# Optimization experiments

Measured on AMD Instinct MI355X. Metric: run time of the kernel, lower is better.

## Reference

```python
import jax, jax.numpy as jnp
import numpy as np

B, ST, SK, D, H, HD, MLP, BLK, NRAND = 2, 2048, 2048, 512, 8, 64, 2048, 64, 3


def _bigbird_block_mask(nq, nk, r, rng):
    """Block-level BigBird mask: 3-block window + global first/last blocks + r random blocks/row."""
    bm = np.zeros((nq, nk), dtype=bool)
    for i in range(nq):
        bm[i, max(i - 1, 0):min(i + 2, nk)] = True  # sliding window of 3 blocks
    bm[0, :] = True; bm[-1, :] = True              # global query blocks
    bm[:, 0] = True; bm[:, -1] = True              # global key blocks
    for i in range(nq):
        avail = np.where(~bm[i])[0]
        if avail.size:
            bm[i, rng.choice(avail, size=min(r, avail.size), replace=False)] = True
    return bm


def _masks():
    rng = np.random.RandomState(0)  # connectivity_seed = 0
    nb_q, nb_k = ST // BLK, SK // BLK
    self_bm = _bigbird_block_mask(nb_q, nb_q, NRAND, rng)
    cross_bm = _bigbird_block_mask(nb_q, nb_k, NRAND, rng)
    ones_blk = np.ones((BLK, BLK), dtype=bool)
    self_mask = np.kron(self_bm, ones_blk) & np.tril(np.ones((ST, ST), dtype=bool))  # causal self-attn
    cross_mask = np.kron(cross_bm, ones_blk)
    return jnp.asarray(self_mask), jnp.asarray(cross_mask)


def setup_inputs() -> dict:
    key = jax.random.key(0)
    ks = jax.random.split(key, 12)
    sd = np.float32(1.0 / np.sqrt(D))
    sh = np.float32(1.0 / np.sqrt(H * HD))
    sm = np.float32(1.0 / np.sqrt(MLP))
    self_mask, cross_mask = _masks()
    return dict(
        targets=jax.random.normal(ks[0], (B, ST, D), jnp.float32),
        encoded=jax.random.normal(ks[1], (B, SK, D), jnp.float32),
        ln1_scale=jnp.ones((D,), jnp.float32), ln1_bias=jnp.zeros((D,), jnp.float32),
        ln2_scale=jnp.ones((D,), jnp.float32), ln2_bias=jnp.zeros((D,), jnp.float32),
        ln3_scale=jnp.ones((D,), jnp.float32), ln3_bias=jnp.zeros((D,), jnp.float32),
        wq1=jax.random.normal(ks[2], (D, H, HD), jnp.float32) * sd,
        wk1=jax.random.normal(ks[3], (D, H, HD), jnp.float32) * sd,
        wv1=jax.random.normal(ks[4], (D, H, HD), jnp.float32) * sd,
        wo1=jax.random.normal(ks[5], (H, HD, D), jnp.float32) * sh,
        wq2=jax.random.normal(ks[6], (D, H, HD), jnp.float32) * sd,
        wk2=jax.random.normal(ks[7], (D, H, HD), jnp.float32) * sd,
        wv2=jax.random.normal(ks[8], (D, H, HD), jnp.float32) * sd,
        wo2=jax.random.normal(ks[9], (H, HD, D), jnp.float32) * sh,
        mlp_w1=jax.random.normal(ks[10], (D, MLP), jnp.float32) * sd,
        mlp_b1=jnp.zeros((MLP,), jnp.float32),
        mlp_w2=jax.random.normal(ks[11], (MLP, D), jnp.float32) * sm,
        mlp_b2=jnp.zeros((D,), jnp.float32),
        self_mask=self_mask, cross_mask=cross_mask,
    )


def _ln(x, s, b, eps=1e-6):
    mu = jnp.mean(x, axis=-1, keepdims=True)
    var = jnp.mean(jnp.square(x - mu), axis=-1, keepdims=True)
    return (x - mu) * jax.lax.rsqrt(var + eps) * s + b


def _attn(xq, xkv, wq, wk, wv, wo, mask):
    q = jnp.einsum('bsd,dhk->bshk', xq, wq) * np.float32(1.0 / np.sqrt(HD))
    k = jnp.einsum('bsd,dhk->bshk', xkv, wk)
    v = jnp.einsum('bsd,dhk->bshk', xkv, wv)
    scores = jnp.einsum('bqhd,bkhd->bhqk', q, k)
    scores = jnp.where(mask[None, None], scores, jnp.float32(-1e9))
    w = jax.nn.softmax(scores, axis=-1)
    o = jnp.einsum('bhqk,bkhd->bqhd', w, v)
    return jnp.einsum('bqhd,hdo->bqo', o, wo)


def reference(targets, encoded, ln1_scale, ln1_bias, ln2_scale, ln2_bias, ln3_scale, ln3_bias,
              wq1, wk1, wv1, wo1, wq2, wk2, wv2, wo2,
              mlp_w1, mlp_b1, mlp_w2, mlp_b2, self_mask, cross_mask):
    # causal BigBird self-attention + residual
    x = _ln(targets, ln1_scale, ln1_bias)
    x = _attn(x, x, wq1, wk1, wv1, wo1, self_mask) + targets
    # BigBird cross-attention over encoder output + residual
    y = _ln(x, ln2_scale, ln2_bias)
    y = _attn(y, encoded, wq2, wk2, wv2, wo2, cross_mask) + x
    # MLP block + residual
    z = _ln(y, ln3_scale, ln3_bias)
    z = jax.nn.gelu(z @ mlp_w1 + mlp_b1) @ mlp_w2 + mlp_b2
    return y + z
```

## Files before the change

kernel.cpp:

```cpp
#include <hip/hip_runtime.h>
#include <hip/hip_bf16.h>

#define DEVINL __device__ __forceinline__

namespace {

constexpr int kB = 2, kST = 2048, kSK = 2048, kD = 512, kH = 8, kHD = 64, kMLP = 2048, kBLK = 64;
constexpr int kNBQ = kST / kBLK;
constexpr int kNBK = kSK / kBLK;
constexpr int kROWS = kB * kST;

typedef float f32x4 __attribute__((ext_vector_type(4)));
typedef int i32x4 __attribute__((ext_vector_type(4)));
typedef short bf16x8 __attribute__((ext_vector_type(8)));

DEVINL float bf2f(unsigned short u) { return __uint_as_float(((unsigned)u) << 16); }

DEVINL unsigned short f2bf(float f) {
  __hip_bfloat16 h = __float2bfloat16(f);
  return *reinterpret_cast<unsigned short*>(&h);
}

DEVINL f32x4 mfma16(bf16x8 a, bf16x8 b, f32x4 c) {
  return __builtin_amdgcn_mfma_f32_16x16x32_bf16(a, b, c, 0, 0, 0);
}

DEVINL int swzb(int r) { return (((r & 7) ^ ((r >> 3) & 7)) << 4); }

__global__ __launch_bounds__(256) void tobf_kernel(const void* __restrict__ src, unsigned short* __restrict__ dst,
                                                   int n8, const unsigned* __restrict__ probe) {
  const bool bf = (probe[0] == 0x3F803F80u);
  const int stride = gridDim.x * blockDim.x;
  if (bf) {
    const i32x4* s = (const i32x4*)src;
    i32x4* d = (i32x4*)dst;
    for (int i = blockIdx.x * blockDim.x + threadIdx.x; i < n8; i += stride) d[i] = s[i];
  } else {
    const f32x4* s = (const f32x4*)src;
    i32x4* d = (i32x4*)dst;
    for (int i = blockIdx.x * blockDim.x + threadIdx.x; i < n8; i += stride) {
      const f32x4 a = s[2 * i], c = s[2 * i + 1];
      union { i32x4 v; unsigned short u[8]; } pk;
#pragma unroll
      for (int j = 0; j < 4; j++) { pk.u[j] = f2bf(a[j]); pk.u[4 + j] = f2bf(c[j]); }
      d[i] = pk.v;
    }
  }
}

struct PSrc { const void* s[8]; };
__global__ __launch_bounds__(256) void param_cvt_kernel(PSrc ps, float* __restrict__ dst,
                                                        const unsigned* __restrict__ probe) {
  const bool bf = (probe[0] == 0x3F803F80u);
  const int i = blockIdx.x * blockDim.x + threadIdx.x;
  if (i >= 5632) return;
  int seg, off;
  if (i < 3072) { seg = i >> 9; off = i & 511; }
  else if (i < 5120) { seg = 6; off = i - 3072; }
  else { seg = 7; off = i - 5120; }
  dst[i] = bf ? bf2f(((const unsigned short*)ps.s[seg])[off]) : ((const float*)ps.s[seg])[off];
}

struct TDesc { const void* src; unsigned short* dst; int K, N, start; float alpha; };
struct TPack { TDesc d[10]; };

__global__ __launch_bounds__(256) void transpose_batch_kernel(TPack p, const unsigned* __restrict__ probe) {
  __shared__ float tile[32][33];
  const bool bf = (probe[0] == 0x3F803F80u);
  const int bid = blockIdx.x;
  int di = 0;
#pragma unroll
  for (int i = 1; i < 10; i++)
    if (bid >= p.d[i].start) di = i;
  const TDesc dd = p.d[di];
  const int local = bid - dd.start;
  const int gx = dd.N / 32;
  const int bx = (local % gx) * 32;
  const int by = (local / gx) * 32;
  const int tx = threadIdx.x & 31, ty = threadIdx.x >> 5;
#pragma unroll
  for (int j = 0; j < 4; j++) {
    const int kr = by + ty + j * 8;
    float v;
    if (bf) v = bf2f(((const unsigned short*)dd.src)[(size_t)kr * dd.N + bx + tx]);
    else v = ((const float*)dd.src)[(size_t)kr * dd.N + bx + tx];
    tile[ty + j * 8][tx] = v;
  }
  __syncthreads();
#pragma unroll
  for (int j = 0; j < 4; j++) {
    const int nr = bx + ty + j * 8;
    dd.dst[(size_t)nr * dd.K + by + tx] = f2bf(dd.alpha * tile[tx][ty + j * 8]);
  }
}

DEVINL int mask_fmt(const void* self_mask) {
  const unsigned* sw = (const unsigned*)self_mask;
  unsigned w = sw[32256];
  unsigned w0 = sw[0];
  if (w == 0x01010101u) return 0;
  if (w0 == 0x3F800000u) return 2;
  if (w0 == 0x00003F80u) return 3;
  return 1;
}

DEVINL bool mask_at(const void* m, int r, int c, int fmt) {
  size_t idx = (size_t)r * kSK + c;
  switch (fmt) {
    case 0: return ((const unsigned char*)m)[idx] != 0;
    case 2: return ((const float*)m)[idx] != 0.f;
    case 3: return ((const unsigned short*)m)[idx] != 0;
    default: return ((const int*)m)[idx] != 0;
  }
}

__global__ void mask_kernel(const void* __restrict__ smask, const void* __restrict__ cmask,
                            unsigned char* __restrict__ sbm, unsigned char* __restrict__ cbm) {
  int fmt = mask_fmt(smask);
  int t = blockIdx.x * blockDim.x + threadIdx.x;
  if (t < kNBQ * kNBK) {
    int i = t / kNBK, j = t % kNBK;
    sbm[t] = mask_at(smask, i * kBLK + kBLK - 1, j * kBLK, fmt) ? 1 : 0;
    cbm[t] = mask_at(cmask, i * kBLK, j * kBLK, fmt) ? 1 : 0;
  }
}

__global__ __launch_bounds__(256) void ln_kernel(const void* __restrict__ x, const float* __restrict__ s,
                                                 const float* __restrict__ b, unsigned short* __restrict__ out,
                                                 int raw, const unsigned* __restrict__ probe) {
  const int row = blockIdx.x, t = threadIdx.x;
  float v0, v1;
  if (raw && probe[0] == 0x3F803F80u) {
    const unsigned u = ((const unsigned*)x)[(size_t)row * 256 + t];
    v0 = bf2f((unsigned short)u);
    v1 = bf2f((unsigned short)(u >> 16));
  } else {
    const float2 f = ((const float2*)x)[(size_t)row * 256 + t];
    v0 = f.x; v1 = f.y;
  }
  float sum = v0 + v1;
#pragma unroll
  for (int o = 32; o; o >>= 1) sum += __shfl_xor(sum, o);
  __shared__ float red[4], red2[4];
  const int wid = t >> 6, lane = t & 63;
  if (lane == 0) red[wid] = sum;
  __syncthreads();
  const float mu = (red[0] + red[1] + red[2] + red[3]) * (1.f / 512.f);
  float d0 = v0 - mu, d1 = v1 - mu;
  float vs = d0 * d0 + d1 * d1;
#pragma unroll
  for (int o = 32; o; o >>= 1) vs += __shfl_xor(vs, o);
  if (lane == 0) red2[wid] = vs;
  __syncthreads();
  const float rstd = rsqrtf((red2[0] + red2[1] + red2[2] + red2[3]) * (1.f / 512.f) + 1e-6f);
  const float o0 = d0 * rstd * s[2 * t] + b[2 * t];
  const float o1 = d1 * rstd * s[2 * t + 1] + b[2 * t + 1];
  ((unsigned*)out)[(size_t)row * 256 + t] = (unsigned)f2bf(o0) | ((unsigned)f2bf(o1) << 16);
}

DEVINL float gelu_f(float x) {
  float u = 0.7978845608028654f * (x + 0.044715f * x * x * x);
  return 0.5f * x * (1.f + tanhf(u));
}

enum { GEPI_QKV = 0, GEPI_BF16 = 1, GEPI_RESID_RAW = 2, GEPI_RESID = 3, GEPI_GELU = 4, GEPI_FINAL = 5 };

template <int BM, int WM, int WN, int MT, int NT, int EPI>
__global__ __launch_bounds__(256) void mfma_gemm_kernel(
    const unsigned short* __restrict__ A, const unsigned short* __restrict__ Bt,
    void* __restrict__ Cout, int M, int N, int K,
    const float* __restrict__ bias, const void* __restrict__ resid,
    const unsigned* __restrict__ probe) {
  __shared__ __align__(16) unsigned short As[2][BM * 64];
  __shared__ __align__(16) unsigned short Bs[2][128 * 64];
  const int t = threadIdx.x, w = t >> 6, lane = t & 63;
  const int lg = lane >> 4, lc = lane & 15;
  const int wm = w / WN, wn = w % WN;
  const int bm = blockIdx.y * BM, bn = blockIdx.x * 128;

  f32x4 acc[MT][NT];
#pragma unroll
  for (int mt = 0; mt < MT; mt++)
#pragma unroll
    for (int nt = 0; nt < NT; nt++) acc[mt][nt] = f32x4{0.f, 0.f, 0.f, 0.f};

  constexpr int AU = BM / 32;
  const int row0 = t >> 3, part16 = (t & 7) * 16;

  i32x4 ar[AU], br[4];
  auto LOADR = [&](int k0) {
#pragma unroll
    for (int i = 0; i < AU; i++) ar[i] = *(const i32x4*)(A + (size_t)(bm + row0 + i * 32) * K + k0 + (part16 >> 1));
#pragma unroll
    for (int i = 0; i < 4; i++) br[i] = *(const i32x4*)(Bt + (size_t)(bn + row0 + i * 32) * K + k0 + (part16 >> 1));
  };
  auto WRITES = [&](int buf) {
#pragma unroll
    for (int i = 0; i < AU; i++) {
      const int r = row0 + i * 32;
      *(i32x4*)((char*)&As[buf][0] + r * 128 + (part16 ^ swzb(r))) = ar[i];
    }
#pragma unroll
    for (int i = 0; i < 4; i++) {
      const int r = row0 + i * 32;
      *(i32x4*)((char*)&Bs[buf][0] + r * 128 + (part16 ^ swzb(r))) = br[i];
    }
  };
  auto COMPUTE = [&](int buf) {
#pragma unroll
    for (int c = 0; c < 2; c++) {
      bf16x8 af[MT], bfv[NT];
#pragma unroll
      for (int mt = 0; mt < MT; mt++) {
        const int r = wm * (MT * 16) + mt * 16 + lc;
        af[mt] = *(const bf16x8*)((const char*)&As[buf][0] + r * 128 + ((c * 64 + lg * 16) ^ swzb(r)));
      }
#pragma unroll
      for (int nt = 0; nt < NT; nt++) {
        const int r = wn * (NT * 16) + nt * 16 + lc;
        bfv[nt] = *(const bf16x8*)((const char*)&Bs[buf][0] + r * 128 + ((c * 64 + lg * 16) ^ swzb(r)));
      }
#pragma unroll
      for (int mt = 0; mt < MT; mt++)
#pragma unroll
        for (int nt = 0; nt < NT; nt++) acc[mt][nt] = mfma16(af[mt], bfv[nt], acc[mt][nt]);
    }
  };

  LOADR(0);
  WRITES(0);
  for (int k0 = 0; k0 < K; k0 += 128) {
    __syncthreads();
    LOADR(k0 + 64);
    COMPUTE(0);
    WRITES(1);
    __syncthreads();
    if (k0 + 128 < K) LOADR(k0 + 128);
    COMPUTE(1);
    if (k0 + 128 < K) WRITES(0);
  }

  bool prb = false;
  if constexpr (EPI == GEPI_FINAL || EPI == GEPI_RESID_RAW) prb = (probe[0] == 0x3F803F80u);
#pragma unroll
  for (int mt = 0; mt < MT; mt++) {
#pragma unroll
    for (int i = 0; i < 4; i++) {
      const int row = bm + wm * (MT * 16) + mt * 16 + lg * 4 + i;
#pragma unroll
      for (int nt = 0; nt < NT; nt++) {
        const int col = bn + wn * (NT * 16) + nt * 16 + lc;
        const float vv = acc[mt][nt][i];
        const size_t idx = (size_t)row * N + col;
        if constexpr (EPI == GEPI_QKV) {
          ((unsigned short*)Cout)[(size_t)(col >> 9) * kROWS * 512 + (size_t)row * 512 + (col & 511)] = f2bf(vv);
        } else if constexpr (EPI == GEPI_BF16) {
          ((unsigned short*)Cout)[idx] = f2bf(vv);
        } else if constexpr (EPI == GEPI_RESID_RAW) {
          const float rv = prb ? bf2f(((const unsigned short*)resid)[idx]) : ((const float*)resid)[idx];
          ((float*)Cout)[idx] = vv + rv;
        } else if constexpr (EPI == GEPI_RESID) {
          ((float*)Cout)[idx] = vv + ((const float*)resid)[idx];
        } else if constexpr (EPI == GEPI_GELU) {
          ((unsigned short*)Cout)[idx] = f2bf(gelu_f(vv + bias[col]));
        } else {
          const float r = vv + bias[col] + ((const float*)resid)[idx];
          if (prb) ((unsigned short*)Cout)[idx] = f2bf(r);
          else ((float*)Cout)[idx] = r;
        }
      }
    }
  }
}

template <bool CAUSAL>
__global__ __launch_bounds__(256) void attn_part_kernel(
    const unsigned short* __restrict__ q, const unsigned short* __restrict__ k,
    const unsigned short* __restrict__ v, const unsigned char* __restrict__ bm,
    unsigned short* __restrict__ o, float* __restrict__ opart,
    float* __restrict__ mpart, float* __restrict__ lpart) {
  __shared__ __align__(16) char smem[16384];
  const int x = blockIdx.x;
  const int s = x & 3, b = (x >> 2) & 1, qb = x >> 3;
  const int h = blockIdx.y;
  const int t = threadIdx.x, w = t >> 6, lane = t & 63;
  const int lg = lane >> 4, lc = lane & 15;

  const unsigned char* bmrow = bm + qb * kNBK;
  const unsigned mask = (unsigned)__ballot(lane < kNBK ? (bmrow[lane] != 0) : false);
  const int cnt = __popc(mask);
  const bool direct = (cnt <= 8);
  if (direct && s > 0) return;
  int lo, hi;
  if (direct) { lo = 0; hi = cnt; }
  else { lo = (s * cnt) >> 2; hi = ((s + 1) * cnt) >> 2; }
  unsigned mrem = mask;
  for (int i = 0; i < lo; i++) mrem &= mrem - 1;
  const int left = hi - lo;

  const size_t qbase = (((size_t)b * kST + qb * 64 + w * 16 + lc) * kH + h) * kHD;
  const bf16x8 aq0 = *(const bf16x8*)(q + qbase + 8 * lg);
  const bf16x8 aq1 = *(const bf16x8*)(q + qbase + 32 + 8 * lg);

  f32x4 ob[4];
#pragma unroll
  for (int dt = 0; dt < 4; dt++) ob[dt] = f32x4{0.f, 0.f, 0.f, 0.f};
  float mi = -1e30f, li = 0.f;

  char* ksb = smem;
  char* vtb = smem + 8192;

  const int krr = t >> 3, kc16 = (t & 7) * 16;
  const int vkvp = t >> 3, vdc = (t & 7) * 8;
  const int vposb = ((vkvp >> 4) << 6) + (((vkvp >> 1) & 3) << 4) + (((vkvp >> 3) & 1) << 3) + ((vkvp & 1) << 2);

  i32x4 kr0, kr1, vr0, vr1;
  auto LOADT = [&](int j) {
    const size_t kb = (((size_t)b * kSK + j * 64) * kH + h) * kHD;
    kr0 = *(const i32x4*)(k + kb + (size_t)krr * (kH * kHD) + (kc16 >> 1));
    kr1 = *(const i32x4*)(k + kb + (size_t)(krr + 32) * (kH * kHD) + (kc16 >> 1));
    vr0 = *(const i32x4*)(v + kb + (size_t)(2 * vkvp) * (kH * kHD) + vdc);
    vr1 = *(const i32x4*)(v + kb + (size_t)(2 * vkvp + 1) * (kH * kHD) + vdc);
  };
  auto WRITET = [&]() {
    *(i32x4*)(ksb + krr * 128 + (kc16 ^ swzb(krr))) = kr0;
    *(i32x4*)(ksb + (krr + 32) * 128 + (kc16 ^ swzb(krr + 32))) = kr1;
    union { i32x4 v4; unsigned short u[8]; } a0, a1;
    a0.v4 = vr0; a1.v4 = vr1;
#pragma unroll
    for (int jj = 0; jj < 8; jj++) {
      const int d = vdc + jj;
      const unsigned val = (unsigned)a0.u[jj] | ((unsigned)a1.u[jj] << 16);
      *(unsigned*)(vtb + d * 128 + (vposb ^ swzb(d))) = val;
    }
  };

  int jcur = (int)__builtin_ctz(mrem);
  mrem &= mrem - 1;
  LOADT(jcur);
  WRITET();
  for (int r = 0; r < left; r++) {
    int jnext = -1;
    if (r + 1 < left) { jnext = (int)__builtin_ctz(mrem); mrem &= mrem - 1; }
    __syncthreads();
    if (jnext >= 0) LOADT(jnext);

    f32x4 sv[4];
#pragma unroll
    for (int t4 = 0; t4 < 4; t4++) sv[t4] = f32x4{0.f, 0.f, 0.f, 0.f};
#pragma unroll
    for (int c = 0; c < 2; c++) {
      const bf16x8 aqc = c ? aq1 : aq0;
#pragma unroll
      for (int t4 = 0; t4 < 4; t4++) {
        const int row = t4 * 16 + lc;
        bf16x8 bk = *(const bf16x8*)(ksb + row * 128 + ((c * 64 + lg * 16) ^ swzb(row)));
        sv[t4] = mfma16(bk, aqc, sv[t4]);
      }
    }

    if (CAUSAL && jcur == qb) {
#pragma unroll
      for (int t4 = 0; t4 < 4; t4++)
#pragma unroll
        for (int i = 0; i < 4; i++)
          if (t4 * 16 + lg * 4 + i > w * 16 + lc) sv[t4][i] = -1e30f;
    }

    float pm = sv[0][0];
#pragma unroll
    for (int t4 = 0; t4 < 4; t4++)
#pragma unroll
      for (int i = 0; i < 4; i++) pm = fmaxf(pm, sv[t4][i]);
    pm = fmaxf(pm, __shfl_xor(pm, 16));
    pm = fmaxf(pm, __shfl_xor(pm, 32));
    const float mn = fmaxf(mi, pm);
    const float corr = __expf(mi - mn);
    mi = mn;
    float rs = 0.f;
#pragma unroll
    for (int t4 = 0; t4 < 4; t4++)
#pragma unroll
      for (int i = 0; i < 4; i++) {
        sv[t4][i] = __expf(sv[t4][i] - mn);
        rs += sv[t4][i];
      }
    rs += __shfl_xor(rs, 16);
    rs += __shfl_xor(rs, 32);
    li = li * corr + rs;

    float cb[4];
#pragma unroll
    for (int i = 0; i < 4; i++) cb[i] = __shfl(corr, lg * 4 + i);
#pragma unroll
    for (int dt = 0; dt < 4; dt++)
#pragma unroll
      for (int i = 0; i < 4; i++) ob[dt][i] *= cb[i];

    bf16x8 pa[2];
#pragma unroll
    for (int c = 0; c < 2; c++) {
      union { bf16x8 v8; unsigned short u[8]; } pk;
#pragma unroll
      for (int jj = 0; jj < 8; jj++) pk.u[jj] = f2bf(sv[2 * c + (jj >> 2)][jj & 3]);
      pa[c] = pk.v8;
    }
#pragma unroll
    for (int c = 0; c < 2; c++)
#pragma unroll
      for (int dt = 0; dt < 4; dt++) {
        const int row = dt * 16 + lc;
        bf16x8 bv = *(const bf16x8*)(vtb + row * 128 + ((c * 64 + lg * 16) ^ swzb(row)));
        ob[dt] = mfma16(pa[c], bv, ob[dt]);
      }

    __syncthreads();
    if (jnext >= 0) WRITET();
    jcur = jnext;
  }

  if (direct) {
    const float linv = 1.0f / li;
    float inv[4];
#pragma unroll
    for (int i = 0; i < 4; i++) inv[i] = __shfl(linv, lg * 4 + i);
    const size_t obase = (((size_t)b * kST + qb * 64 + w * 16) * kH + h) * kHD;
#pragma unroll
    for (int dt = 0; dt < 4; dt++)
#pragma unroll
      for (int i = 0; i < 4; i++)
        o[obase + (size_t)(lg * 4 + i) * (kH * kHD) + dt * 16 + lc] = f2bf(ob[dt][i] * inv[i]);
  } else {
    const int pidx = (((b * kNBQ + qb) * kH) + h) * 4 + s;
    float* op = opart + (size_t)pidx * 4096;
#pragma unroll
    for (int dt = 0; dt < 4; dt++)
#pragma unroll
      for (int i = 0; i < 4; i++)
        op[(w * 16 + lg * 4 + i) * 64 + dt * 16 + lc] = ob[dt][i];
    if (lg == 0) {
      mpart[pidx * 64 + w * 16 + lc] = mi;
      lpart[pidx * 64 + w * 16 + lc] = li;
    }
  }
}

__global__ __launch_bounds__(256) void attn_comb_kernel(
    const unsigned char* __restrict__ bm, const float* __restrict__ opart,
    const float* __restrict__ mpart, const float* __restrict__ lpart,
    unsigned short* __restrict__ o) {
  const int x = blockIdx.x;
  const int qb = x >> 1, b = x & 1, h = blockIdx.y;
  const int t = threadIdx.x, lane = t & 63;
  const unsigned char* bmrow = bm + qb * kNBK;
  const unsigned mask = (unsigned)__ballot(lane < kNBK ? (bmrow[lane] != 0) : false);
  if (__popc(mask) <= 8) return;
  const int base = (((b * kNBQ + qb) * kH) + h) * 4;
  const int r = t >> 2, cg = (t & 3) * 16;
  float m[4], l[4];
#pragma unroll
  for (int s = 0; s < 4; s++) {
    m[s] = mpart[(base + s) * 64 + r];
    l[s] = lpart[(base + s) * 64 + r];
  }
  float M = fmaxf(fmaxf(m[0], m[1]), fmaxf(m[2], m[3]));
  float wgt[4], L = 0.f;
#pragma unroll
  for (int s = 0; s < 4; s++) {
    wgt[s] = __expf(m[s] - M);
    L += l[s] * wgt[s];
  }
  const float inv = 1.f / L;
  const size_t ob_ = (((size_t)b * kST + qb * 64 + r) * kH + h) * kHD + cg;
#pragma unroll
  for (int c = 0; c < 16; c++) {
    float val = 0.f;
#pragma unroll
    for (int s = 0; s < 4; s++) val += opart[(size_t)(base + s) * 4096 + r * 64 + cg + c] * wgt[s];
    o[ob_ + c] = f2bf(val * inv);
  }
}

}

extern "C" void kernel_launch(void* const* d_in, const int* in_sizes, int n_in,
                              void* d_out, int out_size, void* d_ws, size_t ws_size,
                              hipStream_t stream) {
  (void)in_sizes; (void)n_in; (void)out_size; (void)ws_size;
  const unsigned* probe = (const unsigned*)d_in[2];

  char* W = (char*)d_ws;
  size_t off = 0;
  auto allocb = [&](size_t bytes) { char* p = W + off; off += (bytes + 255) & ~size_t(255); return p; };

  float* xbuf = (float*)allocb((size_t)kROWS * kD * 4);
  float* ybuf = (float*)allocb((size_t)kROWS * kD * 4);
  float* f_par = (float*)allocb(5632 * 4);
  float* f_ln[6];
  for (int i = 0; i < 6; i++) f_ln[i] = f_par + i * 512;
  float* f_b1 = f_par + 3072;
  float* f_b2 = f_par + 5120;
  unsigned short* encb = (unsigned short*)allocb((size_t)kROWS * kD * 2);
  unsigned short* lnb  = (unsigned short*)allocb((size_t)kROWS * kD * 2);
  unsigned short* qkvb = (unsigned short*)allocb((size_t)3 * kROWS * kD * 2);
  unsigned short* q2b  = (unsigned short*)allocb((size_t)kROWS * kD * 2);
  unsigned short* kv2b = (unsigned short*)allocb((size_t)2 * kROWS * kD * 2);
  unsigned short* aob  = (unsigned short*)allocb((size_t)kROWS * kD * 2);
  unsigned short* hb16 = (unsigned short*)allocb((size_t)kROWS * kMLP * 2);
  unsigned short* wqkv1 = (unsigned short*)allocb((size_t)3 * 512 * 512 * 2);
  unsigned short* wo1t  = (unsigned short*)allocb((size_t)512 * 512 * 2);
  unsigned short* wq2t  = (unsigned short*)allocb((size_t)512 * 512 * 2);
  unsigned short* wkv2  = (unsigned short*)allocb((size_t)2 * 512 * 512 * 2);
  unsigned short* wo2t  = (unsigned short*)allocb((size_t)512 * 512 * 2);
  unsigned short* w1t   = (unsigned short*)allocb((size_t)2048 * 512 * 2);
  unsigned short* w2t   = (unsigned short*)allocb((size_t)512 * 2048 * 2);
  unsigned char* sbm = (unsigned char*)allocb(kNBQ * kNBK);
  unsigned char* cbm = (unsigned char*)allocb(kNBQ * kNBK);
  float* opart = (float*)allocb((size_t)512 * 4 * 4096 * 4);
  float* mpart = (float*)allocb((size_t)512 * 4 * 64 * 4);
  float* lpart = (float*)allocb((size_t)512 * 4 * 64 * 4);

  tobf_kernel<<<1024, 256, 0, stream>>>(d_in[1], encb, kROWS * kD / 8, probe);
  {
    PSrc ps;
    for (int i = 0; i < 6; i++) ps.s[i] = d_in[2 + i];
    ps.s[6] = d_in[17];
    ps.s[7] = d_in[19];
    param_cvt_kernel<<<22, 256, 0, stream>>>(ps, f_par, probe);
  }
  {
    TPack p;
    const void* srcs[10] = {d_in[8], d_in[9], d_in[10], d_in[11], d_in[12],
                            d_in[13], d_in[14], d_in[15], d_in[16], d_in[18]};
    unsigned short* dsts[10] = {wqkv1, wqkv1 + 512 * 512, wqkv1 + 2 * 512 * 512, wo1t, wq2t,
                                wkv2, wkv2 + 512 * 512, wo2t, w1t, w2t};
    const int Ksz[10] = {512, 512, 512, 512, 512, 512, 512, 512, 512, 2048};
    const int Nsz[10] = {512, 512, 512, 512, 512, 512, 512, 512, 2048, 512};
    int start = 0;
    for (int i = 0; i < 10; i++) {
      p.d[i].src = srcs[i]; p.d[i].dst = dsts[i]; p.d[i].K = Ksz[i]; p.d[i].N = Nsz[i];
      p.d[i].start = start;
      p.d[i].alpha = (i == 0 || i == 4) ? 0.125f : 1.0f;
      start += (Nsz[i] / 32) * (Ksz[i] / 32);
    }
    transpose_batch_kernel<<<start, 256, 0, stream>>>(p, probe);
  }
  mask_kernel<<<1, 1024, 0, stream>>>(d_in[20], d_in[21], sbm, cbm);

  const dim3 blk(256);
  const dim3 g_qkv1(12, 32);
  const dim3 g_kv2(8, 32);
  const dim3 g_mlp1(16, 32);
  const dim3 g_n512(4, 64);
  const dim3 g_attnp(kNBQ * kB * 4, kH);
  const dim3 g_attnc(kNBQ * kB, kH);

  unsigned short* qb16 = qkvb;
  unsigned short* kb16 = qkvb + (size_t)kROWS * 512;
  unsigned short* vb16 = qkvb + (size_t)2 * kROWS * 512;
  unsigned short* k2b = kv2b;
  unsigned short* v2b = kv2b + (size_t)kROWS * 512;

  ln_kernel<<<kROWS, blk, 0, stream>>>(d_in[0], f_ln[0], f_ln[1], lnb, 1, probe);
  mfma_gemm_kernel<128, 2, 2, 4, 4, GEPI_QKV><<<g_qkv1, blk, 0, stream>>>(lnb, wqkv1, qkvb, kROWS, 1536, 512, nullptr, nullptr, probe);
  attn_part_kernel<true><<<g_attnp, blk, 0, stream>>>(qb16, kb16, vb16, sbm, aob, opart, mpart, lpart);
  attn_comb_kernel<<<g_attnc, blk, 0, stream>>>(sbm, opart, mpart, lpart, aob);
  mfma_gemm_kernel<64, 1, 4, 4, 2, GEPI_RESID_RAW><<<g_n512, blk, 0, stream>>>(aob, wo1t, xbuf, kROWS, 512, 512, nullptr, d_in[0], probe);

  ln_kernel<<<kROWS, blk, 0, stream>>>(xbuf, f_ln[2], f_ln[3], lnb, 0, probe);
  mfma_gemm_kernel<64, 1, 4, 4, 2, GEPI_BF16><<<g_n512, blk, 0, stream>>>(lnb, wq2t, q2b, kROWS, 512, 512, nullptr, nullptr, probe);
  mfma_gemm_kernel<128, 2, 2, 4, 4, GEPI_QKV><<<g_kv2, blk, 0, stream>>>(encb, wkv2, kv2b, kROWS, 1024, 512, nullptr, nullptr, probe);
  attn_part_kernel<false><<<g_attnp, blk, 0, stream>>>(q2b, k2b, v2b, cbm, aob, opart, mpart, lpart);
  attn_comb_kernel<<<g_attnc, blk, 0, stream>>>(cbm, opart, mpart, lpart, aob);
  mfma_gemm_kernel<64, 1, 4, 4, 2, GEPI_RESID><<<g_n512, blk, 0, stream>>>(aob, wo2t, ybuf, kROWS, 512, 512, nullptr, xbuf, probe);

  ln_kernel<<<kROWS, blk, 0, stream>>>(ybuf, f_ln[4], f_ln[5], lnb, 0, probe);
  mfma_gemm_kernel<128, 2, 2, 4, 4, GEPI_GELU><<<g_mlp1, blk, 0, stream>>>(lnb, w1t, hb16, kROWS, kMLP, 512, f_b1, nullptr, probe);
  mfma_gemm_kernel<64, 1, 4, 4, 2, GEPI_FINAL><<<g_n512, blk, 0, stream>>>(hb16, w2t, d_out, kROWS, 512, 2048, f_b2, ybuf, probe);
}
```

Before: 234.0 us.

## Store QKV head-major and fuse cross-attention Q and KV projections

The QKV projection epilogue now writes Q/K/V in a [batch, head, seq, 64] layout, so each attention tile's K and V loads read one contiguous 8 KB chunk instead of strided rows. The cross-attention Q projection (from the layer-norm output) and the KV projection (from the encoder) are merged into one GEMM launch that picks the A operand per column block, with the weights packed into a single buffer. This cuts one launch and improves the coalescing of attention loads. In exchange, the GEMM epilogue does more scattered stores and needs extra index arithmetic.

```diff
diff --git a/kernel.cpp b/kernel.cpp
--- a/kernel.cpp
+++ b/kernel.cpp
@@ -163,11 +163,12 @@
   return 0.5f * x * (1.f + tanhf(u));
 }
 
-enum { GEPI_QKV = 0, GEPI_BF16 = 1, GEPI_RESID_RAW = 2, GEPI_RESID = 3, GEPI_GELU = 4, GEPI_FINAL = 5 };
+enum { GEPI_QKV = 0, GEPI_QKV2 = 1, GEPI_RESID_RAW = 2, GEPI_RESID = 3, GEPI_GELU = 4, GEPI_FINAL = 5 };
 
 template <int BM, int WM, int WN, int MT, int NT, int EPI>
 __global__ __launch_bounds__(256) void mfma_gemm_kernel(
-    const unsigned short* __restrict__ A, const unsigned short* __restrict__ Bt,
+    const unsigned short* __restrict__ A, const unsigned short* __restrict__ A2,
+    const unsigned short* __restrict__ Bt,
     void* __restrict__ Cout, int M, int N, int K,
     const float* __restrict__ bias, const void* __restrict__ resid,
     const unsigned* __restrict__ probe) {
@@ -178,6 +179,11 @@
   const int wm = w / WN, wn = w % WN;
   const int bm = blockIdx.y * BM, bn = blockIdx.x * 128;
 
+  const unsigned short* Aop = A;
+  if constexpr (EPI == GEPI_QKV2) {
+    if (bn >= 512) Aop = A2;
+  }
+
   f32x4 acc[MT][NT];
 #pragma unroll
   for (int mt = 0; mt < MT; mt++)
@@ -190,7 +196,7 @@
   i32x4 ar[AU], br[4];
   auto LOADR = [&](int k0) {
 #pragma unroll
-    for (int i = 0; i < AU; i++) ar[i] = *(const i32x4*)(A + (size_t)(bm + row0 + i * 32) * K + k0 + (part16 >> 1));
+    for (int i = 0; i < AU; i++) ar[i] = *(const i32x4*)(Aop + (size_t)(bm + row0 + i * 32) * K + k0 + (part16 >> 1));
 #pragma unroll
     for (int i = 0; i < 4; i++) br[i] = *(const i32x4*)(Bt + (size_t)(bn + row0 + i * 32) * K + k0 + (part16 >> 1));
   };
@@ -252,10 +258,11 @@
         const int col = bn + wn * (NT * 16) + nt * 16 + lc;
         const float vv = acc[mt][nt][i];
         const size_t idx = (size_t)row * N + col;
-        if constexpr (EPI == GEPI_QKV) {
-          ((unsigned short*)Cout)[(size_t)(col >> 9) * kROWS * 512 + (size_t)row * 512 + (col & 511)] = f2bf(vv);
-        } else if constexpr (EPI == GEPI_BF16) {
-          ((unsigned short*)Cout)[idx] = f2bf(vv);
+        if constexpr (EPI == GEPI_QKV || EPI == GEPI_QKV2) {
+          const int bb = row >> 11, ss = row & 2047;
+          const int hh = (col >> 6) & 7, hd = col & 63;
+          ((unsigned short*)Cout)[(size_t)(col >> 9) * kROWS * 512 +
+                                  (((size_t)bb * kH + hh) * kST + ss) * 64 + hd] = f2bf(vv);
         } else if constexpr (EPI == GEPI_RESID_RAW) {
           const float rv = prb ? bf2f(((const unsigned short*)resid)[idx]) : ((const float*)resid)[idx];
           ((float*)Cout)[idx] = vv + rv;
@@ -298,7 +305,8 @@
   for (int i = 0; i < lo; i++) mrem &= mrem - 1;
   const int left = hi - lo;
 
-  const size_t qbase = (((size_t)b * kST + qb * 64 + w * 16 + lc) * kH + h) * kHD;
+  const size_t hbase = ((size_t)b * kH + h) * kST;
+  const size_t qbase = (hbase + qb * 64 + w * 16 + lc) * 64;
   const bf16x8 aq0 = *(const bf16x8*)(q + qbase + 8 * lg);
   const bf16x8 aq1 = *(const bf16x8*)(q + qbase + 32 + 8 * lg);
 
@@ -316,11 +324,12 @@
 
   i32x4 kr0, kr1, vr0, vr1;
   auto LOADT = [&](int j) {
-    const size_t kb = (((size_t)b * kSK + j * 64) * kH + h) * kHD;
-    kr0 = *(const i32x4*)(k + kb + (size_t)krr * (kH * kHD) + (kc16 >> 1));
-    kr1 = *(const i32x4*)(k + kb + (size_t)(krr + 32) * (kH * kHD) + (kc16 >> 1));
-    vr0 = *(const i32x4*)(v + kb + (size_t)(2 * vkvp) * (kH * kHD) + vdc);
-    vr1 = *(const i32x4*)(v + kb + (size_t)(2 * vkvp + 1) * (kH * kHD) + vdc);
+    const unsigned short* kb = k + (hbase + j * 64) * 64;
+    kr0 = *(const i32x4*)(kb + t * 8);
+    kr1 = *(const i32x4*)(kb + 2048 + t * 8);
+    const unsigned short* vb = v + (hbase + j * 64) * 64;
+    vr0 = *(const i32x4*)(vb + (2 * vkvp) * 64 + vdc);
+    vr1 = *(const i32x4*)(vb + (2 * vkvp + 1) * 64 + vdc);
   };
   auto WRITET = [&]() {
     *(i32x4*)(ksb + krr * 128 + (kc16 ^ swzb(krr))) = kr0;
@@ -503,14 +512,12 @@
   unsigned short* encb = (unsigned short*)allocb((size_t)kROWS * kD * 2);
   unsigned short* lnb  = (unsigned short*)allocb((size_t)kROWS * kD * 2);
   unsigned short* qkvb = (unsigned short*)allocb((size_t)3 * kROWS * kD * 2);
-  unsigned short* q2b  = (unsigned short*)allocb((size_t)kROWS * kD * 2);
-  unsigned short* kv2b = (unsigned short*)allocb((size_t)2 * kROWS * kD * 2);
+  unsigned short* qkv2 = (unsigned short*)allocb((size_t)3 * kROWS * kD * 2);
   unsigned short* aob  = (unsigned short*)allocb((size_t)kROWS * kD * 2);
   unsigned short* hb16 = (unsigned short*)allocb((size_t)kROWS * kMLP * 2);
   unsigned short* wqkv1 = (unsigned short*)allocb((size_t)3 * 512 * 512 * 2);
+  unsigned short* wqkv2 = (unsigned short*)allocb((size_t)3 * 512 * 512 * 2);
   unsigned short* wo1t  = (unsigned short*)allocb((size_t)512 * 512 * 2);
-  unsigned short* wq2t  = (unsigned short*)allocb((size_t)512 * 512 * 2);
-  unsigned short* wkv2  = (unsigned short*)allocb((size_t)2 * 512 * 512 * 2);
   unsigned short* wo2t  = (unsigned short*)allocb((size_t)512 * 512 * 2);
   unsigned short* w1t   = (unsigned short*)allocb((size_t)2048 * 512 * 2);
   unsigned short* w2t   = (unsigned short*)allocb((size_t)512 * 2048 * 2);
@@ -530,17 +537,19 @@
   }
   {
     TPack p;
-    const void* srcs[10] = {d_in[8], d_in[9], d_in[10], d_in[11], d_in[12],
-                            d_in[13], d_in[14], d_in[15], d_in[16], d_in[18]};
-    unsigned short* dsts[10] = {wqkv1, wqkv1 + 512 * 512, wqkv1 + 2 * 512 * 512, wo1t, wq2t,
-                                wkv2, wkv2 + 512 * 512, wo2t, w1t, w2t};
+    const void* srcs[10] = {d_in[8], d_in[9], d_in[10],
+                            d_in[12], d_in[13], d_in[14],
+                            d_in[11], d_in[15], d_in[16], d_in[18]};
+    unsigned short* dsts[10] = {wqkv1, wqkv1 + 512 * 512, wqkv1 + 2 * 512 * 512,
+                                wqkv2, wqkv2 + 512 * 512, wqkv2 + 2 * 512 * 512,
+                                wo1t, wo2t, w1t, w2t};
     const int Ksz[10] = {512, 512, 512, 512, 512, 512, 512, 512, 512, 2048};
     const int Nsz[10] = {512, 512, 512, 512, 512, 512, 512, 512, 2048, 512};
     int start = 0;
     for (int i = 0; i < 10; i++) {
       p.d[i].src = srcs[i]; p.d[i].dst = dsts[i]; p.d[i].K = Ksz[i]; p.d[i].N = Nsz[i];
       p.d[i].start = start;
-      p.d[i].alpha = (i == 0 || i == 4) ? 0.125f : 1.0f;
+      p.d[i].alpha = (i == 0 || i == 3) ? 0.125f : 1.0f;
       start += (Nsz[i] / 32) * (Ksz[i] / 32);
     }
     transpose_batch_kernel<<<start, 256, 0, stream>>>(p, probe);
@@ -548,8 +557,7 @@
   mask_kernel<<<1, 1024, 0, stream>>>(d_in[20], d_in[21], sbm, cbm);
 
   const dim3 blk(256);
-  const dim3 g_qkv1(12, 32);
-  const dim3 g_kv2(8, 32);
+  const dim3 g_qkv(12, 32);
   const dim3 g_mlp1(16, 32);
   const dim3 g_n512(4, 64);
   const dim3 g_attnp(kNBQ * kB * 4, kH);
@@ -558,23 +566,23 @@
   unsigned short* qb16 = qkvb;
   unsigned short* kb16 = qkvb + (size_t)kROWS * 512;
   unsigned short* vb16 = qkvb + (size_t)2 * kROWS * 512;
-  unsigned short* k2b = kv2b;
-  unsigned short* v2b = kv2b + (size_t)kROWS * 512;
+  unsigned short* q2b = qkv2;
+  unsigned short* k2b = qkv2 + (size_t)kROWS * 512;
+  unsigned short* v2b = qkv2 + (size_t)2 * kROWS * 512;
 
   ln_kernel<<<kROWS, blk, 0, stream>>>(d_in[0], f_ln[0], f_ln[1], lnb, 1, probe);
-  mfma_gemm_kernel<128, 2, 2, 4, 4, GEPI_QKV><<<g_qkv1, blk, 0, stream>>>(lnb, wqkv1, qkvb, kROWS, 1536, 512, nullptr, nullptr, probe);
+  mfma_gemm_kernel<128, 2, 2, 4, 4, GEPI_QKV><<<g_qkv, blk, 0, stream>>>(lnb, nullptr, wqkv1, qkvb, kROWS, 1536, 512, nullptr, nullptr, probe);
   attn_part_kernel<true><<<g_attnp, blk, 0, stream>>>(qb16, kb16, vb16, sbm, aob, opart, mpart, lpart);
   attn_comb_kernel<<<g_attnc, blk, 0, stream>>>(sbm, opart, mpart, lpart, aob);
-  mfma_gemm_kernel<64, 1, 4, 4, 2, GEPI_RESID_RAW><<<g_n512, blk, 0, stream>>>(aob, wo1t, xbuf, kROWS, 512, 512, nullptr, d_in[0], probe);
+  mfma_gemm_kernel<64, 1, 4, 4, 2, GEPI_RESID_RAW><<<g_n512, blk, 0, stream>>>(aob, nullptr, wo1t, xbuf, kROWS, 512, 512, nullptr, d_in[0], probe);
 
   ln_kernel<<<kROWS, blk, 0, stream>>>(xbuf, f_ln[2], f_ln[3], lnb, 0, probe);
-  mfma_gemm_kernel<64, 1, 4, 4, 2, GEPI_BF16><<<g_n512, blk, 0, stream>>>(lnb, wq2t, q2b, kROWS, 512, 512, nullptr, nullptr, probe);
-  mfma_gemm_kernel<128, 2, 2, 4, 4, GEPI_QKV><<<g_kv2, blk, 0, stream>>>(encb, wkv2, kv2b, kROWS, 1024, 512, nullptr, nullptr, probe);
+  mfma_gemm_kernel<128, 2, 2, 4, 4, GEPI_QKV2><<<g_qkv, blk, 0, stream>>>(lnb, encb, wqkv2, qkv2, kROWS, 1536, 512, nullptr, nullptr, probe);
   attn_part_kernel<false><<<g_attnp, blk, 0, stream>>>(q2b, k2b, v2b, cbm, aob, opart, mpart, lpart);
   attn_comb_kernel<<<g_attnc, blk, 0, stream>>>(cbm, opart, mpart, lpart, aob);
-  mfma_gemm_kernel<64, 1, 4, 4, 2, GEPI_RESID><<<g_n512, blk, 0, stream>>>(aob, wo2t, ybuf, kROWS, 512, 512, nullptr, xbuf, probe);
+  mfma_gemm_kernel<64, 1, 4, 4, 2, GEPI_RESID><<<g_n512, blk, 0, stream>>>(aob, nullptr, wo2t, ybuf, kROWS, 512, 512, nullptr, xbuf, probe);
 
   ln_kernel<<<kROWS, blk, 0, stream>>>(ybuf, f_ln[4], f_ln[5], lnb, 0, probe);
-  mfma_gemm_kernel<128, 2, 2, 4, 4, GEPI_GELU><<<g_mlp1, blk, 0, stream>>>(lnb, w1t, hb16, kROWS, kMLP, 512, f_b1, nullptr, probe);
-  mfma_gemm_kernel<64, 1, 4, 4, 2, GEPI_FINAL><<<g_n512, blk, 0, stream>>>(hb16, w2t, d_out, kROWS, 512, 2048, f_b2, ybuf, probe);
-}
+  mfma_gemm_kernel<128, 2, 2, 4, 4, GEPI_GELU><<<g_mlp1, blk, 0, stream>>>(lnb, nullptr, w1t, hb16, kROWS, kMLP, 512, f_b1, nullptr, probe);
+  mfma_gemm_kernel<64, 1, 4, 4, 2, GEPI_FINAL><<<g_n512, blk, 0, stream>>>(hb16, nullptr, w2t, d_out, kROWS, 512, 2048, f_b2, ybuf, probe);
+}
```

After: 227.0 us. -3.0%, faster.
